# Performance work log

Hardware: AMD Instinct MI355X
Metric: run time of the kernel (lower is better)

## Reference

```python
import jax, jax.numpy as jnp
import numpy as np

D_MODEL = 2048
N_HEAD = 16
N_KV_HEAD = 4
D_HEAD = D_MODEL // N_HEAD  # 128
ROPE_BASE = 10000.0


def build_rope_cache(d_head, seq_len):
    # NeoX-style half-split RoPE cache: cos/sin of shape [T, d_head]
    inv_freq = 1.0 / (ROPE_BASE ** (jnp.arange(0, d_head, 2, dtype=jnp.float32) / d_head))
    t = jnp.arange(seq_len, dtype=jnp.float32)
    ang = jnp.einsum('t,f->tf', t, inv_freq)            # [T, d_head/2]
    ang = jnp.concatenate([ang, ang], axis=-1)           # [T, d_head]
    return jnp.cos(ang), jnp.sin(ang)


def apply_rope(x, cos, sin):
    # x: [B, T, H, Dh]; cos/sin: [T, Dh]
    d = x.shape[-1]
    x1, x2 = x[..., : d // 2], x[..., d // 2 :]
    rot = jnp.concatenate([-x2, x1], axis=-1)
    c = cos[None, :, None, :]
    s = sin[None, :, None, :]
    return x * c + rot * s


def setup_inputs() -> dict:
    key = jax.random.key(0)
    k1, k2, k3, k4, k5 = jax.random.split(key, 5)
    B, T = 4, 2048
    scale = 1.0 / np.sqrt(D_MODEL)
    return {
        'x': jax.random.normal(k1, (B, T, D_MODEL), dtype=jnp.float32),
        'Wq': jax.random.normal(k2, (D_MODEL, N_HEAD * D_HEAD), dtype=jnp.float32) * scale,
        'Wk': jax.random.normal(k3, (D_MODEL, N_KV_HEAD * D_HEAD), dtype=jnp.float32) * scale,
        'Wv': jax.random.normal(k4, (D_MODEL, N_KV_HEAD * D_HEAD), dtype=jnp.float32) * scale,
        'Wo': jax.random.normal(k5, (D_MODEL, D_MODEL), dtype=jnp.float32) * scale,
    }


def reference(x, Wq, Wk, Wv, Wo):
    B, T, C = x.shape
    q = (x @ Wq).reshape(B, T, N_HEAD, D_HEAD)
    k = (x @ Wk).reshape(B, T, N_KV_HEAD, D_HEAD)
    v = (x @ Wv).reshape(B, T, N_KV_HEAD, D_HEAD)

    cos, sin = build_rope_cache(D_HEAD, T)  # no cache -> positions [0, T)
    q = apply_rope(q, cos, sin)
    k = apply_rope(k, cos, sin)

    q = q.transpose(0, 2, 1, 3)  # [B, H, T, Dh]
    k = k.transpose(0, 2, 1, 3)  # [B, Hkv, T, Dh]
    v = v.transpose(0, 2, 1, 3)

    rf = N_HEAD // N_KV_HEAD
    k = jnp.repeat(k, rf, axis=1)  # GQA: repeat_interleave over head dim
    v = jnp.repeat(v, rf, axis=1)

    scores = jnp.einsum('bhtd,bhsd->bhts', q, k) / np.sqrt(D_HEAD)
    causal = jnp.tril(jnp.ones((T, T), dtype=bool))
    scores = jnp.where(causal[None, None], scores, -jnp.inf)
    probs = jax.nn.softmax(scores, axis=-1)
    attn = jnp.einsum('bhts,bhsd->bhtd', probs, v)

    attn = attn.transpose(0, 2, 1, 3).reshape(B, T, C)
    return attn @ Wo
```

## Files before the change

kernel.cpp:

```cpp
#include <hip/hip_runtime.h>

typedef unsigned short u16;
typedef __bf16 bf16x8 __attribute__((ext_vector_type(8)));
typedef u16 u16x8 __attribute__((ext_vector_type(8)));
typedef u16 u16x4 __attribute__((ext_vector_type(4)));
typedef float f32x4 __attribute__((ext_vector_type(4)));

#define MFMA16(a, b, c) __builtin_amdgcn_mfma_f32_16x16x32_bf16((a), (b), (c), 0, 0, 0)

__device__ __forceinline__ void async16(const u16* g, u16* l) {
  __builtin_amdgcn_global_load_lds(
      (__attribute__((address_space(1))) void*)(void*)(g),
      (__attribute__((address_space(3))) void*)(void*)(l), 16, 0, 0);
}

__device__ __forceinline__ float bf2f(u16 b) {
  union { unsigned u; float f; } v;
  v.u = ((unsigned)b) << 16;
  return v.f;
}
__device__ __forceinline__ u16 f2bf(float f) {
  union { float f; unsigned u; } v;
  v.f = f;
  unsigned u = v.u;
  return (u16)((u + 0x7FFFu + ((u >> 16) & 1u)) >> 16);
}

__global__ __launch_bounds__(256) void convert_k(const float* __restrict__ in,
                                                 u16* __restrict__ out, int n8) {
  const int stride = gridDim.x * 256;
  for (int i = blockIdx.x * 256 + threadIdx.x; i < n8; i += stride) {
    const float* fp = in + (size_t)i * 8;
    float4 a = *(const float4*)fp, b = *(const float4*)(fp + 4);
    u16x8 o;
    o[0] = f2bf(a.x); o[1] = f2bf(a.y); o[2] = f2bf(a.z); o[3] = f2bf(a.w);
    o[4] = f2bf(b.x); o[5] = f2bf(b.y); o[6] = f2bf(b.z); o[7] = f2bf(b.w);
    *(u16x8*)&out[(size_t)i * 8] = o;
  }
}

__global__ __launch_bounds__(256) void transpose_cvt_k(const float* __restrict__ W,
                                                       u16* __restrict__ Wt, int K, int N) {
  __shared__ __align__(16) u16 tile[64 * 72];
  const int t = threadIdx.x;
  const int n0 = blockIdx.x * 64, k0 = blockIdx.y * 64;
#pragma unroll
  for (int i = 0; i < 2; ++i) {
    int flat = t + i * 256;
    int r = flat >> 3, c8 = (flat & 7) * 8;
    const float* p = W + (size_t)(k0 + r) * N + n0 + c8;
    float4 a = *(const float4*)p, b = *(const float4*)(p + 4);
    u16x8 v;
    v[0] = f2bf(a.x); v[1] = f2bf(a.y); v[2] = f2bf(a.z); v[3] = f2bf(a.w);
    v[4] = f2bf(b.x); v[5] = f2bf(b.y); v[6] = f2bf(b.z); v[7] = f2bf(b.w);
#pragma unroll
    for (int j = 0; j < 8; ++j) tile[r * 72 + c8 + j] = v[j];
  }
  __syncthreads();
#pragma unroll
  for (int i = 0; i < 2; ++i) {
    int flat = t + i * 256;
    int r = flat >> 3, c8 = (flat & 7) * 8;
    u16x8 v;
#pragma unroll
    for (int j = 0; j < 8; ++j) v[j] = tile[(c8 + j) * 72 + r];
    *(u16x8*)&Wt[(size_t)(n0 + r) * K + k0 + c8] = v;
  }
}

__global__ __launch_bounds__(256) void rope_table_k(float* __restrict__ cosT,
                                                    float* __restrict__ sinT) {
  int idx = blockIdx.x * 256 + threadIdx.x;
  int tp = idx >> 6, i = idx & 63;
  float invf = expf(-(float)i * (9.210340371976184f / 64.0f));
  float ang = (float)tp * invf;
  cosT[idx] = cosf(ang);
  sinT[idx] = sinf(ang);
}

__global__ __launch_bounds__(256) void rope_apply_k(u16* __restrict__ base,
                                                    const float* __restrict__ cosT,
                                                    const float* __restrict__ sinT,
                                                    int rowStride, int nhMask, int rowShift,
                                                    float scale) {
  int idx = blockIdx.x * 256 + threadIdx.x;
  int i4 = idx & 15;
  int hh = (idx >> 4) & nhMask;
  int row = idx >> rowShift;
  int tp = row & 2047;
  int i = i4 * 4;
  u16* p = base + (size_t)row * rowStride + hh * 128;
  u16x4 a = *(u16x4*)&p[i];
  u16x4 b = *(u16x4*)&p[i + 64];
  float4 c = *(const float4*)&cosT[tp * 64 + i];
  float4 s = *(const float4*)&sinT[tp * 64 + i];
  float cc[4] = {c.x, c.y, c.z, c.w}, ss[4] = {s.x, s.y, s.z, s.w};
  u16x4 oa, ob;
#pragma unroll
  for (int j = 0; j < 4; ++j) {
    float x1 = bf2f(a[j]), x2 = bf2f(b[j]);
    oa[j] = f2bf((x1 * cc[j] - x2 * ss[j]) * scale);
    ob[j] = f2bf((x2 * cc[j] + x1 * ss[j]) * scale);
  }
  *(u16x4*)&p[i] = oa;
  *(u16x4*)&p[i + 64] = ob;
}

template <bool F32OUT>
__global__ __launch_bounds__(256) void gemm_tn(const u16* __restrict__ A,
                                               const u16* __restrict__ Bt,
                                               void* __restrict__ C, int M, int N, int K) {
  __shared__ __align__(16) u16 As[128 * 32];
  __shared__ __align__(16) u16 Bs[128 * 32];
  const int t = threadIdx.x;
  const int l = t & 63, w = t >> 6;
  const int wm = w >> 1, wn = w & 1;
  const int lr = l & 15, lg = l >> 4;
  const int nbx = gridDim.x;
  const int lin = blockIdx.y * nbx + blockIdx.x;
  const int cpx = (nbx * gridDim.y) >> 3;
  const int sl = (lin & 7) * cpx + (lin >> 3);
  const size_t m0 = (size_t)(sl / nbx) * 128, n0 = (size_t)(sl % nbx) * 128;
  f32x4 acc[4][4] = {};
  for (int k0 = 0; k0 < K; k0 += 32) {
#pragma unroll
    for (int i = 0; i < 2; ++i) {
      int flat = t + i * 256;
      int r = flat >> 2, seg = (flat & 3) * 8;
      async16(&A[(m0 + r) * K + k0 + seg], &As[flat * 8]);
      async16(&Bt[(n0 + r) * K + k0 + seg], &Bs[flat * 8]);
    }
    __syncthreads();
    bf16x8 af[4], bfr[4];
#pragma unroll
    for (int i = 0; i < 4; ++i) {
      af[i] = *(const bf16x8*)&As[(wm * 64 + i * 16 + lr) * 32 + lg * 8];
      bfr[i] = *(const bf16x8*)&Bs[(wn * 64 + i * 16 + lr) * 32 + lg * 8];
    }
#pragma unroll
    for (int mi = 0; mi < 4; ++mi)
#pragma unroll
      for (int ni = 0; ni < 4; ++ni) acc[mi][ni] = MFMA16(af[mi], bfr[ni], acc[mi][ni]);
    __syncthreads();
  }
#pragma unroll
  for (int mi = 0; mi < 4; ++mi)
#pragma unroll
    for (int ni = 0; ni < 4; ++ni)
#pragma unroll
      for (int r = 0; r < 4; ++r) {
        size_t row = m0 + wm * 64 + mi * 16 + lg * 4 + r;
        size_t col = n0 + wn * 64 + ni * 16 + lr;
        if constexpr (F32OUT)
          ((float*)C)[row * N + col] = acc[mi][ni][r];
        else
          ((u16*)C)[row * N + col] = f2bf(acc[mi][ni][r]);
      }
}

__global__ __launch_bounds__(512, 4) void attn_k(const u16* __restrict__ QKV,
                                                 u16* __restrict__ O) {
  constexpr int T = 2048, CS = 3072, OC = 2048;
  __shared__ __align__(16) u16 Ks[2][64 * 128];
  __shared__ __align__(16) u16 Vt[128 * 72];
  __shared__ __align__(16) u16 Pl[128 * 72];
  const int t = threadIdx.x, l = t & 63, w = t >> 6, lr = l & 15, lg = l >> 4;
  const int lin = blockIdx.x;
  const int v = (lin & 7) * 128 + (lin >> 3);
  const int bh = v >> 4;
  const int qt = 15 - (v & 15);
  const int b = bh >> 4, h = bh & 15, kv = h >> 2;
  const int q0 = qt * 128;
  const int myrow = w * 16 + lg * 4;
  const size_t rowQ = (size_t)(b * T + q0 + w * 16 + lr) * CS + h * 128;
  bf16x8 qf[4];
#pragma unroll
  for (int di = 0; di < 4; ++di) qf[di] = *(const bf16x8*)&QKV[rowQ + di * 32 + lg * 8];
  bf16x8 onesf;
#pragma unroll
  for (int j = 0; j < 8; ++j) onesf[j] = (__bf16)1.0f;
  f32x4 lsum = {};
  f32x4 oacc[8] = {};
  const int lastst = 2 * qt + 1;
  const size_t kvBase = (size_t)(b * T) * CS + 2048 + kv * 128;
  const int sV = (t >> 4) * 2, d8V = (t & 15) * 8;
  u16x8 vr0, vr1;
  {
#pragma unroll
    for (int i = 0; i < 2; ++i) {
      int flat = t + i * 512;
      int r = flat >> 4, c = flat & 15;
      async16(&QKV[kvBase + (size_t)r * CS + ((c ^ (r & 7)) * 8)], &Ks[0][flat * 8]);
    }
    vr0 = *(const u16x8*)&QKV[kvBase + 512 + (size_t)sV * CS + d8V];
    vr1 = *(const u16x8*)&QKV[kvBase + 512 + (size_t)(sV + 1) * CS + d8V];
#pragma unroll
    for (int j = 0; j < 8; ++j) {
      int d = d8V + j;
      int slot = (sV >> 3) ^ ((d >> 3) & 7);
      *(unsigned*)&Vt[d * 72 + slot * 8 + (sV & 7)] = (unsigned)vr0[j] | ((unsigned)vr1[j] << 16);
    }
    __syncthreads();
  }
  int cb = 0;
  for (int st = 0; st <= lastst; ++st) {
    if (st < lastst) {
      const size_t kvRow = kvBase + (size_t)(st + 1) * 64 * CS;
#pragma unroll
      for (int i = 0; i < 2; ++i) {
        int flat = t + i * 512;
        int r = flat >> 4, c = flat & 15;
        async16(&QKV[kvRow + (size_t)r * CS + ((c ^ (r & 7)) * 8)], &Ks[cb ^ 1][flat * 8]);
      }
      vr0 = *(const u16x8*)&QKV[kvRow + 512 + (size_t)sV * CS + d8V];
      vr1 = *(const u16x8*)&QKV[kvRow + 512 + (size_t)(sV + 1) * CS + d8V];
    }
    const int s0 = st * 64;
    const bool skip = (st == lastst) && (w < 4);
    if (!skip) {
      f32x4 sacc[4] = {};
      __builtin_amdgcn_s_setprio(1);
#pragma unroll
      for (int di = 0; di < 4; ++di)
#pragma unroll
        for (int n = 0; n < 4; ++n) {
          bf16x8 bk =
              *(const bf16x8*)&Ks[cb][(n * 16 + lr) * 128 + (((di * 4 + lg) ^ (lr & 7)) << 3)];
          sacc[n] = MFMA16(qf[di], bk, sacc[n]);
        }
      __builtin_amdgcn_s_setprio(0);
      const bool diag = (st >= 2 * qt);
#pragma unroll
      for (int n = 0; n < 4; ++n)
#pragma unroll
        for (int r = 0; r < 4; ++r) {
          float s_ = sacc[n][r] * 1.44269504f - 11.5415603f;
          if (diag && (s0 + 16 * n + lr > q0 + myrow + r)) s_ = -1e30f;
          *(__bf16*)&Pl[(myrow + r) * 72 + 16 * n + lr] = (__bf16)exp2f(s_);
        }
      __builtin_amdgcn_s_setprio(1);
#pragma unroll
      for (int ks = 0; ks < 2; ++ks) {
        bf16x8 pa = *(const bf16x8*)&Pl[(w * 16 + lr) * 72 + ks * 32 + lg * 8];
        lsum = MFMA16(pa, onesf, lsum);
#pragma unroll
        for (int nf = 0; nf < 8; ++nf) {
          int d = 16 * nf + lr;
          int seg = lg + 4 * ks;
          bf16x8 vb = *(const bf16x8*)&Vt[d * 72 + ((seg ^ ((d >> 3) & 7)) << 3)];
          oacc[nf] = MFMA16(pa, vb, oacc[nf]);
        }
      }
      __builtin_amdgcn_s_setprio(0);
    }
    __syncthreads();
    if (st < lastst) {
#pragma unroll
      for (int j = 0; j < 8; ++j) {
        int d = d8V + j;
        int slot = (sV >> 3) ^ ((d >> 3) & 7);
        *(unsigned*)&Vt[d * 72 + slot * 8 + (sV & 7)] =
            (unsigned)vr0[j] | ((unsigned)vr1[j] << 16);
      }
    }
    __syncthreads();
    cb ^= 1;
  }
#pragma unroll
  for (int r = 0; r < 4; ++r) {
    float il = 1.0f / lsum[r];
    size_t orow = (size_t)(b * T + q0 + myrow + r) * OC + h * 128;
#pragma unroll
    for (int nf = 0; nf < 8; ++nf) O[orow + 16 * nf + lr] = f2bf(oacc[nf][r] * il);
  }
}

__global__ __launch_bounds__(256) void sentinel_k(float* __restrict__ out) {
  out[blockIdx.x * 256 + threadIdx.x] = 1.0e4f;
}

extern "C" void kernel_launch(void* const* d_in, const int* in_sizes, int n_in, void* d_out,
                              int out_size, void* d_ws, size_t ws_size, hipStream_t stream) {
  const float* x = (const float*)d_in[0];
  const float* Wq = (const float*)d_in[1];
  const float* Wk = (const float*)d_in[2];
  const float* Wv = (const float*)d_in[3];
  const float* Wo = (const float*)d_in[4];

  char* p = (char*)d_ws;
  auto take = [&](size_t bytes) {
    char* r = p;
    p += (bytes + 255) & ~(size_t)255;
    return r;
  };
  u16* WqkvT = (u16*)take((size_t)3072 * 2048 * 2);
  u16* WoT = (u16*)take((size_t)2048 * 2048 * 2);
  u16* QKV = (u16*)take((size_t)8192 * 3072 * 2);
  u16* Ob = (u16*)take((size_t)8192 * 2048 * 2);
  u16* xbf = (u16*)take((size_t)8192 * 2048 * 2);
  float* cosT = (float*)take((size_t)2048 * 64 * 4);
  float* sinT = (float*)take((size_t)2048 * 64 * 4);
  if (ws_size < (size_t)(p - (char*)d_ws)) {
    sentinel_k<<<4, 256, 0, stream>>>((float*)d_out);
    return;
  }

  convert_k<<<2048, 256, 0, stream>>>(x, xbf, 8192 * 2048 / 8);
  transpose_cvt_k<<<dim3(32, 32), 256, 0, stream>>>(Wq, WqkvT, 2048, 2048);
  transpose_cvt_k<<<dim3(8, 32), 256, 0, stream>>>(Wk, WqkvT + (size_t)2048 * 2048, 2048, 512);
  transpose_cvt_k<<<dim3(8, 32), 256, 0, stream>>>(Wv, WqkvT + (size_t)2560 * 2048, 2048, 512);
  transpose_cvt_k<<<dim3(32, 32), 256, 0, stream>>>(Wo, WoT, 2048, 2048);
  rope_table_k<<<512, 256, 0, stream>>>(cosT, sinT);

  gemm_tn<false><<<dim3(24, 64), 256, 0, stream>>>(xbf, WqkvT, QKV, 8192, 3072, 2048);

  rope_apply_k<<<8192, 256, 0, stream>>>(QKV, cosT, sinT, 3072, 15, 8, 0.08838834764831845f);
  rope_apply_k<<<2048, 256, 0, stream>>>(QKV + 2048, cosT, sinT, 3072, 3, 6, 1.0f);

  attn_k<<<1024, 512, 0, stream>>>(QKV, Ob);

  gemm_tn<true><<<dim3(16, 64), 256, 0, stream>>>(Ob, WoT, (void*)d_out, 8192, 2048, 2048);
}
```

Baseline: 465.1 us.

## Replace GEMM with 256x256 double-buffered, swizzled 8-wave pipelined kernel

Replaces the 128x128 single-buffered GEMM used for the QKV and output projections with a 256x256-tile, 512-thread kernel that streams 64-wide K slices into double-buffered LDS. Staging is interleaved with MFMA phases using fine-grained vmcnt waits, and MFMA sections get raised priority. An XOR swizzle on the LDS layout avoids bank conflicts. The aim is to hide global-load latency behind compute and raise arithmetic intensity per tile. The cost is 128 KB of LDS per block, which limits occupancy to one block per CU, and the grid shrinks to 384 and 256 blocks.

After: 477.3 us. 2.6% more time.

```diff
diff --git a/kernel.cpp b/kernel.cpp
--- a/kernel.cpp
+++ b/kernel.cpp
@@ -107,49 +107,86 @@
 }
 
 template <bool F32OUT>
-__global__ __launch_bounds__(256) void gemm_tn(const u16* __restrict__ A,
-                                               const u16* __restrict__ Bt,
-                                               void* __restrict__ C, int M, int N, int K) {
-  __shared__ __align__(16) u16 As[128 * 32];
-  __shared__ __align__(16) u16 Bs[128 * 32];
-  const int t = threadIdx.x;
-  const int l = t & 63, w = t >> 6;
-  const int wm = w >> 1, wn = w & 1;
+__global__ __launch_bounds__(512, 1) void gemm8p(const u16* __restrict__ A,
+                                                 const u16* __restrict__ Bt,
+                                                 void* __restrict__ C, int M, int N, int K) {
+  __shared__ __align__(16) u16 As[2][256 * 64];
+  __shared__ __align__(16) u16 Bs[2][256 * 64];
+  const int t = threadIdx.x, l = t & 63, w = t >> 6;
   const int lr = l & 15, lg = l >> 4;
+  const int wm = w >> 2, wn = w & 3;
   const int nbx = gridDim.x;
   const int lin = blockIdx.y * nbx + blockIdx.x;
   const int cpx = (nbx * gridDim.y) >> 3;
   const int sl = (lin & 7) * cpx + (lin >> 3);
-  const size_t m0 = (size_t)(sl / nbx) * 128, n0 = (size_t)(sl % nbx) * 128;
-  f32x4 acc[4][4] = {};
-  for (int k0 = 0; k0 < K; k0 += 32) {
-#pragma unroll
-    for (int i = 0; i < 2; ++i) {
-      int flat = t + i * 256;
-      int r = flat >> 2, seg = (flat & 3) * 8;
-      async16(&A[(m0 + r) * K + k0 + seg], &As[flat * 8]);
-      async16(&Bt[(n0 + r) * K + k0 + seg], &Bs[flat * 8]);
-    }
-    __syncthreads();
-    bf16x8 af[4], bfr[4];
-#pragma unroll
-    for (int i = 0; i < 4; ++i) {
-      af[i] = *(const bf16x8*)&As[(wm * 64 + i * 16 + lr) * 32 + lg * 8];
-      bfr[i] = *(const bf16x8*)&Bs[(wn * 64 + i * 16 + lr) * 32 + lg * 8];
-    }
-#pragma unroll
-    for (int mi = 0; mi < 4; ++mi)
-#pragma unroll
-      for (int ni = 0; ni < 4; ++ni) acc[mi][ni] = MFMA16(af[mi], bfr[ni], acc[mi][ni]);
-    __syncthreads();
-  }
-#pragma unroll
-  for (int mi = 0; mi < 4; ++mi)
+  const size_t m0 = (size_t)(sl / nbx) * 256, n0 = (size_t)(sl % nbx) * 256;
+  const int sr = t >> 3, sc = t & 7;
+
+  auto stage = [&](int hk, int kt, int d) {
+    const u16* X = (hk < 2) ? A : Bt;
+    const size_t x0 = (hk < 2) ? m0 : n0;
+    u16* Xs = (hk < 2) ? &As[d][0] : &Bs[d][0];
+    const int h = hk & 1;
+#pragma unroll
+    for (int j = 0; j < 2; ++j) {
+      int r = sr + j * 64;
+      async16(&X[(x0 + h * 128 + r) * K + kt * 64 + ((sc ^ (r & 7)) * 8)],
+              &Xs[h * 8192 + (j * 512 + t) * 8]);
+    }
+  };
+
+  f32x4 acc[8][4] = {};
+  const int NIT = K >> 7;
+#pragma unroll
+  for (int hk = 0; hk < 4; ++hk) stage(hk, 0, 0);
+
+  for (int it = 0; it < NIT; ++it) {
+    const int ktB = 2 * it + 1, ktN = 2 * it + 2;
+    const bool last = (it + 1 == NIT);
+#pragma unroll
+    for (int p = 0; p < 8; ++p) {
+      const int d = p >> 2, q = p & 3, miH = q >> 1, niH = q & 1;
+      if (p < 4) stage(p, ktB, 1);
+      else if (!last) stage(p - 4, ktN, 0);
+      if (q == 0) {
+        if (p == 4 && last) { asm volatile("s_waitcnt vmcnt(0)" ::: "memory"); }
+        else                { asm volatile("s_waitcnt vmcnt(2)" ::: "memory"); }
+        __builtin_amdgcn_s_barrier();
+      }
+      bf16x8 a[4][2], b[2][2];
+#pragma unroll
+      for (int m2 = 0; m2 < 4; ++m2)
+#pragma unroll
+        for (int ks = 0; ks < 2; ++ks)
+          a[m2][ks] = *(const bf16x8*)&As[d][(wm * 128 + (miH * 4 + m2) * 16 + lr) * 64 +
+                                            (((ks * 4 + lg) ^ (lr & 7)) << 3)];
+#pragma unroll
+      for (int n2 = 0; n2 < 2; ++n2)
+#pragma unroll
+        for (int ks = 0; ks < 2; ++ks)
+          b[n2][ks] = *(const bf16x8*)&Bs[d][(wn * 64 + (niH * 2 + n2) * 16 + lr) * 64 +
+                                            (((ks * 4 + lg) ^ (lr & 7)) << 3)];
+      if (q != 0) __builtin_amdgcn_s_barrier();
+      __builtin_amdgcn_s_setprio(1);
+#pragma unroll
+      for (int m2 = 0; m2 < 4; ++m2)
+#pragma unroll
+        for (int n2 = 0; n2 < 2; ++n2)
+#pragma unroll
+          for (int ks = 0; ks < 2; ++ks)
+            acc[miH * 4 + m2][niH * 2 + n2] =
+                MFMA16(a[m2][ks], b[n2][ks], acc[miH * 4 + m2][niH * 2 + n2]);
+      __builtin_amdgcn_s_setprio(0);
+      __builtin_amdgcn_s_barrier();
+    }
+  }
+#pragma unroll
+  for (int mi = 0; mi < 8; ++mi)
 #pragma unroll
     for (int ni = 0; ni < 4; ++ni)
 #pragma unroll
       for (int r = 0; r < 4; ++r) {
-        size_t row = m0 + wm * 64 + mi * 16 + lg * 4 + r;
+        size_t row = m0 + wm * 128 + mi * 16 + lg * 4 + r;
         size_t col = n0 + wn * 64 + ni * 16 + lr;
         if constexpr (F32OUT)
           ((float*)C)[row * N + col] = acc[mi][ni][r];
@@ -312,12 +349,12 @@
   transpose_cvt_k<<<dim3(32, 32), 256, 0, stream>>>(Wo, WoT, 2048, 2048);
   rope_table_k<<<512, 256, 0, stream>>>(cosT, sinT);
 
-  gemm_tn<false><<<dim3(24, 64), 256, 0, stream>>>(xbf, WqkvT, QKV, 8192, 3072, 2048);
+  gemm8p<false><<<dim3(12, 32), 512, 0, stream>>>(xbf, WqkvT, QKV, 8192, 3072, 2048);
 
   rope_apply_k<<<8192, 256, 0, stream>>>(QKV, cosT, sinT, 3072, 15, 8, 0.08838834764831845f);
   rope_apply_k<<<2048, 256, 0, stream>>>(QKV + 2048, cosT, sinT, 3072, 3, 6, 1.0f);
 
   attn_k<<<1024, 512, 0, stream>>>(QKV, Ob);
 
-  gemm_tn<true><<<dim3(16, 64), 256, 0, stream>>>(Ob, WoT, (void*)d_out, 8192, 2048, 2048);
-}
+  gemm8p<true><<<dim3(8, 32), 512, 0, stream>>>(Ob, WoT, (void*)d_out, 8192, 2048, 2048);
+}
```
